# Performance work log

Measured on AMD Instinct MI355X. Metric: run time of the kernel, lower is better.

Reference implementation:

```python
import jax, jax.numpy as jnp
import numpy as np

N = 50000        # nodes
E = 800000       # edges (before self-loops)
IN = 128         # in_channels
HID = 256        # hidden_channels
HEADS = 8
C = HID // HEADS # per-head channels = 32
NC = 64          # num_classes
L = 3            # num_layers - 1 hidden GATConv layers


def setup_inputs() -> dict:
    key = jax.random.key(0)
    ks = jax.random.split(key, 12)
    x = jax.random.normal(ks[0], (N, IN), dtype=jnp.float32)
    edge_index = jax.random.randint(ks[1], (2, E), 0, N, dtype=jnp.int64)
    s = 0.05
    W0 = jax.random.normal(ks[2], (IN, HID), jnp.float32) * s
    b0 = jnp.zeros((HID,), jnp.float32)
    Wc = jax.random.normal(ks[3], (L, HID, HID), jnp.float32) * s
    a_src_c = jax.random.normal(ks[4], (L, HEADS, C), jnp.float32) * s
    a_dst_c = jax.random.normal(ks[5], (L, HEADS, C), jnp.float32) * s
    bc = jnp.zeros((L, HID), jnp.float32)
    Wl = jax.random.normal(ks[6], (HID, NC), jnp.float32) * s
    a_src_l = jax.random.normal(ks[7], (1, NC), jnp.float32) * s
    a_dst_l = jax.random.normal(ks[8], (1, NC), jnp.float32) * s
    bl = jnp.zeros((NC,), jnp.float32)
    return {"x": x, "edge_index": edge_index, "W0": W0, "b0": b0,
            "Wc": Wc, "a_src_c": a_src_c, "a_dst_c": a_dst_c, "bc": bc,
            "Wl": Wl, "a_src_l": a_src_l, "a_dst_l": a_dst_l, "bl": bl}


def gat_layer(h_in, W, a_s, a_d, b, src, dst, n, heads, c, concat):
    # PyG GATConv: h = x W -> [n, heads, c]
    h = (h_in @ W).reshape(n, heads, c)
    alpha_s = jnp.einsum('nhc,hc->nh', h, a_s)  # [n, heads]
    alpha_d = jnp.einsum('nhc,hc->nh', h, a_d)
    e = jax.nn.leaky_relu(alpha_s[src] + alpha_d[dst], 0.2)  # [E', heads]
    # scatter-softmax over incoming edges of each destination node
    m = jax.ops.segment_max(e, dst, num_segments=n)
    ex = jnp.exp(e - m[dst])
    den = jax.ops.segment_sum(ex, dst, num_segments=n)
    att = ex / (den[dst] + 1e-16)                            # [E', heads]
    out = jax.ops.segment_sum(h[src] * att[:, :, None], dst, num_segments=n)
    out = out.reshape(n, heads * c) if concat else out.mean(axis=1)
    return out + b


def reference(x, edge_index, W0, b0, Wc, a_src_c, a_dst_c, bc, Wl, a_src_l, a_dst_l, bl):
    n = x.shape[0]
    loops = jnp.arange(n, dtype=edge_index.dtype)
    src = jnp.concatenate([edge_index[0], loops])  # GATConv adds self-loops
    dst = jnp.concatenate([edge_index[1], loops])
    h = x @ W0 + b0                                 # node_embed
    xs = [h]
    for l in range(Wc.shape[0]):
        h = gat_layer(h, Wc[l], a_src_c[l], a_dst_c[l], bc[l], src, dst, n, HEADS, C, True)
        h = jax.nn.relu(h)                          # dropout p=0 (eval)
        xs.append(h)
    out = gat_layer(h, Wl, a_src_l, a_dst_l, bl, src, dst, n, 1, NC, False)
    xs.append(out)
    return jnp.concatenate(xs, axis=-1)             # JumpingKnowledge 'cat'
```

## Files before the change

kernel.cpp:

```cpp
#include <hip/hip_runtime.h>

typedef __attribute__((ext_vector_type(8))) short short8v;
typedef __attribute__((ext_vector_type(4))) float f32x4;

#define IN_CH 128
#define HID   256
#define HEADS 8
#define NCLS  64
#define LDO   1088
#define LDOU  2176

__device__ __forceinline__ unsigned short f2b(float f) {
    unsigned u = __float_as_uint(f);
    u += 0x7FFFu + ((u >> 16) & 1u);
    return (unsigned short)(u >> 16);
}
__device__ __forceinline__ float b2f(unsigned short s) {
    return __uint_as_float(((unsigned)s) << 16);
}

__global__ void detect64(const int* __restrict__ ei, int* __restrict__ flag, int E) {
    __shared__ int nz;
    if (threadIdx.x == 0) nz = 0;
    __syncthreads();
    int v = ei[2 * threadIdx.x + 1];
    if (v != 0) atomicAdd(&nz, 1);
    __syncthreads();
    if (threadIdx.x == 0) flag[0] = (nz == 0) ? 1 : 0;
}

__global__ void hist_k(const int* __restrict__ ei, const int* __restrict__ flag,
                       int* __restrict__ deg, int E) {
    int i = blockIdx.x * 256 + threadIdx.x;
    if (i >= E) return;
    int is64 = flag[0];
    int dst = is64 ? ei[2 * (E + i)] : ei[E + i];
    atomicAdd(&deg[dst], 1);
}

__global__ void scan_k(const int* __restrict__ deg, int* __restrict__ rowptr, int N) {
    __shared__ int sums[1024];
    int t = threadIdx.x;
    int chunk = (N + 1023) >> 10;
    int beg = t * chunk;
    int end = beg + chunk; if (end > N) end = N;
    if (beg > N) beg = N;
    int s = 0;
    for (int i = beg; i < end; ++i) s += deg[i];
    sums[t] = s;
    __syncthreads();
    for (int o = 1; o < 1024; o <<= 1) {
        int v = (t >= o) ? sums[t - o] : 0;
        __syncthreads();
        sums[t] += v;
        __syncthreads();
    }
    int run = (t == 0) ? 0 : sums[t - 1];
    for (int i = beg; i < end; ++i) { rowptr[i] = run; run += deg[i]; }
    if (t == 1023) rowptr[N] = sums[1023];
}

__global__ void fill_k(const int* __restrict__ ei, const int* __restrict__ flag,
                       const int* __restrict__ rowptr, int* __restrict__ cnt,
                       int* __restrict__ colb, int E) {
    int i = blockIdx.x * 256 + threadIdx.x;
    if (i >= E) return;
    int is64 = flag[0];
    int src, dst;
    if (is64) { src = ei[2 * i]; dst = ei[2 * (E + i)]; }
    else      { src = ei[i];     dst = ei[E + i]; }
    int pos = rowptr[dst] + atomicAdd(&cnt[dst], 1);
    colb[pos] = src;
}

__global__ void convtw(const float* __restrict__ W, unsigned short* __restrict__ WT,
                       int K, int N) {
    int i = blockIdx.x * 256 + threadIdx.x;
    if (i >= K * N) return;
    int k = i / N, n = i - k * N;
    WT[(size_t)n * K + k] = f2b(W[i]);
}

#define GBM 128
#define GBN 64
#define GBK 32
#define GLD 56

template<int OUTF32>
__global__ __launch_bounds__(256) void gemm_bf16(
    const float* __restrict__ A, int lda,
    const unsigned short* __restrict__ BT,
    int M, int N, int K,
    float* __restrict__ outF, const float* __restrict__ bias,
    unsigned short* __restrict__ outB, int ostride)
{
    __shared__ unsigned short Asm[GBM][GLD];
    __shared__ unsigned short Bsm[GBN][GLD];
    const int t = threadIdx.x;
    const int wid = t >> 6, lane = t & 63;
    const int m0 = blockIdx.x * GBM;
    const int n0 = blockIdx.y * GBN;
    const int wm = (wid >> 1) * 64;
    const int wn = (wid & 1) * 32;

    f32x4 acc[4][2];
#pragma unroll
    for (int i = 0; i < 4; ++i)
#pragma unroll
        for (int j = 0; j < 2; ++j) acc[i][j] = (f32x4)0.f;

    const int ar = t >> 3;
    const int ac = (t & 7) * 4;
    const int bc_ = t >> 2;
    const int bk = (t & 3) * 8;
    const int kk = (lane >> 4) * 8;
    const int rA = lane & 15;

    for (int k0 = 0; k0 < K; k0 += GBK) {
        __syncthreads();
#pragma unroll
        for (int p = 0; p < 4; ++p) {
            int row = ar + p * 32;
            int grow = m0 + row;
            float4 v = make_float4(0.f, 0.f, 0.f, 0.f);
            if (grow < M) v = *(const float4*)(A + (size_t)grow * lda + k0 + ac);
            ushort4 w4;
            w4.x = f2b(v.x); w4.y = f2b(v.y); w4.z = f2b(v.z); w4.w = f2b(v.w);
            *(ushort4*)&Asm[row][ac] = w4;
        }
        {
            int4 v = *(const int4*)(BT + (size_t)(n0 + bc_) * K + k0 + bk);
            *(int4*)&Bsm[bc_][bk] = v;
        }
        __syncthreads();
        short8v af[4], bfr[2];
#pragma unroll
        for (int i = 0; i < 4; ++i) af[i] = *(const short8v*)&Asm[wm + i * 16 + rA][kk];
#pragma unroll
        for (int j = 0; j < 2; ++j) bfr[j] = *(const short8v*)&Bsm[wn + j * 16 + rA][kk];
#pragma unroll
        for (int i = 0; i < 4; ++i)
#pragma unroll
            for (int j = 0; j < 2; ++j)
                acc[i][j] = __builtin_amdgcn_mfma_f32_16x16x32_bf16(af[i], bfr[j], acc[i][j], 0, 0, 0);
    }

    const int cr = (lane >> 4) * 4;
    const int cc = lane & 15;
#pragma unroll
    for (int i = 0; i < 4; ++i)
#pragma unroll
        for (int j = 0; j < 2; ++j)
#pragma unroll
            for (int r = 0; r < 4; ++r) {
                int row = m0 + wm + i * 16 + cr + r;
                int col = n0 + wn + j * 16 + cc;
                if (row < M) {
                    float v = acc[i][j][r];
                    if (OUTF32) outF[(size_t)row * LDO + col] = v + bias[col];
                    else        outB[(size_t)row * ostride + col] = f2b(v);
                }
            }
}

__global__ void alpha8(const unsigned short* __restrict__ tb, int tstride,
                       const float* __restrict__ as_, const float* __restrict__ ad_,
                       float* __restrict__ aS, float* __restrict__ aD, int n) {
    int wid = threadIdx.x >> 6, lane = threadIdx.x & 63;
    int node = blockIdx.x * 4 + wid;
    if (node >= n) return;
    int c = lane * 4;
    ushort4 hv = *(const ushort4*)(tb + (size_t)node * tstride + c);
    float4 av = *(const float4*)(as_ + c);
    float4 dv = *(const float4*)(ad_ + c);
    float h0 = b2f(hv.x), h1 = b2f(hv.y), h2 = b2f(hv.z), h3 = b2f(hv.w);
    float s = h0 * av.x + h1 * av.y + h2 * av.z + h3 * av.w;
    float d = h0 * dv.x + h1 * dv.y + h2 * dv.z + h3 * dv.w;
    s += __shfl_xor(s, 1); s += __shfl_xor(s, 2); s += __shfl_xor(s, 4);
    d += __shfl_xor(d, 1); d += __shfl_xor(d, 2); d += __shfl_xor(d, 4);
    if ((lane & 7) == 0) {
        aS[node * HEADS + (lane >> 3)] = s;
        aD[node * HEADS + (lane >> 3)] = d;
    }
}

__global__ void alpha1(const unsigned short* __restrict__ tb64, int tstride,
                       const float* __restrict__ as_, const float* __restrict__ ad_,
                       float* __restrict__ aS, float* __restrict__ aD, int n) {
    int wid = threadIdx.x >> 6, lane = threadIdx.x & 63;
    int node = blockIdx.x * 4 + wid;
    if (node >= n) return;
    float v = b2f(tb64[(size_t)node * tstride + lane]);
    float s = v * as_[lane], d = v * ad_[lane];
#pragma unroll
    for (int o = 1; o < 64; o <<= 1) { s += __shfl_xor(s, o); d += __shfl_xor(d, o); }
    if (lane == 0) { aS[node] = s; aD[node] = d; }
}

__global__ void agg8(const int* __restrict__ rowptr, const int* __restrict__ colb,
                     const float* __restrict__ aS, const float* __restrict__ aD,
                     const unsigned short* __restrict__ tb, int tstride,
                     const float* __restrict__ bias,
                     float* __restrict__ outp, int n, int dorelu) {
    int wid = threadIdx.x >> 6, lane = threadIdx.x & 63;
    int node = blockIdx.x * 4 + wid;
    if (node >= n) return;
    int c = lane * 4, head = lane >> 3;
    float aDv = aD[node * HEADS + head];
    float xs = aS[node * HEADS + head] + aDv;
    xs = xs > 0.f ? xs : 0.2f * xs;
    float wS = __expf(xs);
    float den = wS + 1e-16f;
    ushort4 hv0 = *(const ushort4*)(tb + (size_t)node * tstride + c);
    float a0 = wS * b2f(hv0.x), a1 = wS * b2f(hv0.y);
    float a2 = wS * b2f(hv0.z), a3 = wS * b2f(hv0.w);
    int s0 = rowptr[node], s1 = rowptr[node + 1];
    for (int e = s0; e < s1; ++e) {
        int src = colb[e];
        float xx = aS[src * HEADS + head] + aDv;
        xx = xx > 0.f ? xx : 0.2f * xx;
        float w = __expf(xx);
        den += w;
        ushort4 hv = *(const ushort4*)(tb + (size_t)src * tstride + c);
        a0 += w * b2f(hv.x); a1 += w * b2f(hv.y);
        a2 += w * b2f(hv.z); a3 += w * b2f(hv.w);
    }
    float inv = 1.f / den;
    float4 bv = *(const float4*)(bias + c);
    float o0 = a0 * inv + bv.x, o1 = a1 * inv + bv.y;
    float o2 = a2 * inv + bv.z, o3 = a3 * inv + bv.w;
    if (dorelu) {
        o0 = fmaxf(o0, 0.f); o1 = fmaxf(o1, 0.f);
        o2 = fmaxf(o2, 0.f); o3 = fmaxf(o3, 0.f);
    }
    *(float4*)(outp + (size_t)node * LDO + c) = make_float4(o0, o1, o2, o3);
}

__global__ void agg1(const int* __restrict__ rowptr, const int* __restrict__ colb,
                     const float* __restrict__ aS, const float* __restrict__ aD,
                     const unsigned short* __restrict__ tb64, int tstride,
                     const float* __restrict__ bl,
                     float* __restrict__ outp, int n) {
    int wid = threadIdx.x >> 6, lane = threadIdx.x & 63;
    int node = blockIdx.x * 4 + wid;
    if (node >= n) return;
    float aDv = aD[node];
    float xs = aS[node] + aDv;
    xs = xs > 0.f ? xs : 0.2f * xs;
    float wS = __expf(xs);
    float den = wS + 1e-16f;
    float acc = wS * b2f(tb64[(size_t)node * tstride + lane]);
    int s0 = rowptr[node], s1 = rowptr[node + 1];
    for (int e = s0; e < s1; ++e) {
        int src = colb[e];
        float xx = aS[src] + aDv;
        xx = xx > 0.f ? xx : 0.2f * xx;
        float w = __expf(xx);
        den += w;
        acc += w * b2f(tb64[(size_t)src * tstride + lane]);
    }
    outp[(size_t)node * LDO + 1024 + lane] = acc / den + bl[lane];
}

extern "C" void kernel_launch(void* const* d_in, const int* in_sizes, int n_in,
                              void* d_out, int out_size, void* d_ws, size_t ws_size,
                              hipStream_t stream) {
    const float* x   = (const float*)d_in[0];
    const int*   ei  = (const int*)d_in[1];
    const float* W0  = (const float*)d_in[2];
    const float* b0  = (const float*)d_in[3];
    const float* Wc  = (const float*)d_in[4];
    const float* asc = (const float*)d_in[5];
    const float* adc = (const float*)d_in[6];
    const float* bc  = (const float*)d_in[7];
    const float* Wl  = (const float*)d_in[8];
    const float* asl = (const float*)d_in[9];
    const float* adl = (const float*)d_in[10];
    const float* bl  = (const float*)d_in[11];
    float* out = (float*)d_out;
    unsigned short* outU = (unsigned short*)d_out;

    const int N = in_sizes[0] / IN_CH;
    const int E = in_sizes[1] / 2;

    unsigned short* t0 = outU + 896 * 2;
    unsigned short* t1 = outU + 768 * 2;
    unsigned short* t2 = outU;
    unsigned short* tF = outU + 128 * 2;

    char* ws = (char*)d_ws;
    size_t off = 0;
    auto take = [&](size_t bytes) -> void* {
        void* p = ws + off;
        off += (bytes + 255) & ~(size_t)255;
        return p;
    };
    unsigned short* WbT = (unsigned short*)take((size_t)245760 * 2);
    float* aS   = (float*)take((size_t)N * HEADS * 4);
    float* aD   = (float*)take((size_t)N * HEADS * 4);
    int* deg    = (int*)take((size_t)N * 4);
    int* cnt    = (int*)take((size_t)N * 4);
    int* rowptr = (int*)take((size_t)(N + 1) * 4);
    int* colb   = (int*)take((size_t)E * 4);
    int* flag   = (int*)take(256);

    unsigned short* W0T  = WbT;
    unsigned short* WcT0 = WbT + 32768;
    unsigned short* WlT  = WbT + 32768 + 3 * 65536;

    hipMemsetAsync(deg, 0, (size_t)N * 4, stream);
    hipMemsetAsync(cnt, 0, (size_t)N * 4, stream);

    detect64<<<1, 256, 0, stream>>>(ei, flag, E);
    convtw<<<(32768 + 255) / 256, 256, 0, stream>>>(W0, W0T, 128, 256);
    for (int l = 0; l < 3; ++l)
        convtw<<<(65536 + 255) / 256, 256, 0, stream>>>(Wc + l * 65536, WcT0 + l * 65536, 256, 256);
    convtw<<<(16384 + 255) / 256, 256, 0, stream>>>(Wl, WlT, 256, 64);

    hist_k<<<(E + 255) / 256, 256, 0, stream>>>(ei, flag, deg, E);
    scan_k<<<1, 1024, 0, stream>>>(deg, rowptr, N);
    fill_k<<<(E + 255) / 256, 256, 0, stream>>>(ei, flag, rowptr, cnt, colb, E);

    const int gmx = (N + GBM - 1) / GBM;
    const int nwb = (N + 3) / 4;

    gemm_bf16<1><<<dim3(gmx, 4), 256, 0, stream>>>(x, IN_CH, W0T, N, 256, 128, out, b0, nullptr, 0);

    unsigned short* tbs[3] = { t0, t1, t2 };
    for (int l = 0; l < 3; ++l) {
        gemm_bf16<0><<<dim3(gmx, 4), 256, 0, stream>>>(out + 256 * l, LDO, WcT0 + l * 65536,
                                                       N, 256, 256, nullptr, nullptr, tbs[l], LDOU);
        alpha8<<<nwb, 256, 0, stream>>>(tbs[l], LDOU, asc + l * 256, adc + l * 256, aS, aD, N);
        agg8<<<nwb, 256, 0, stream>>>(rowptr, colb, aS, aD, tbs[l], LDOU, bc + l * 256,
                                      out + 256 * (l + 1), N, 1);
    }

    gemm_bf16<0><<<dim3(gmx, 1), 256, 0, stream>>>(out + 768, LDO, WlT, N, 64, 256, nullptr, nullptr, tF, LDOU);
    alpha1<<<nwb, 256, 0, stream>>>(tF, LDOU, asl, adl, aS, aD, N);
    agg1<<<nwb, 256, 0, stream>>>(rowptr, colb, aS, aD, tF, LDOU, bl, out, N);

    gemm_bf16<1><<<dim3(gmx, 4), 256, 0, stream>>>(x, IN_CH, W0T, N, 256, 128, out, b0, nullptr, 0);
}
```

Before: 976.0 us.

## Feed GEMMs bf16 activations staged in output scratch and merge weight conversions

Layer outputs are now also written as bf16 copies into unused regions of the output buffer, and x is pre-converted to bf16, so the hidden-layer GEMMs read half-width bf16 A operands instead of converting fp32 in every tile. The GEMM K-tile is raised from 32 to 64. The five weight-transpose launches are merged into one kernel, and the aggregation loops get unroll hints. This cuts A-operand read traffic and launch count, but adds extra bf16 stores and relies on a careful aliasing plan for the scratch regions inside the output buffer.

Result: faster. 867.4 us (-11.1%).

```diff
diff --git a/kernel.cpp b/kernel.cpp
--- a/kernel.cpp
+++ b/kernel.cpp
@@ -73,24 +73,46 @@
     colb[pos] = src;
 }
 
-__global__ void convtw(const float* __restrict__ W, unsigned short* __restrict__ WT,
-                       int K, int N) {
+__global__ void convw_all(const float* __restrict__ W0, const float* __restrict__ Wc,
+                          const float* __restrict__ Wl,
+                          unsigned short* __restrict__ W0T, unsigned short* __restrict__ WcT,
+                          unsigned short* __restrict__ WlT) {
     int i = blockIdx.x * 256 + threadIdx.x;
-    if (i >= K * N) return;
-    int k = i / N, n = i - k * N;
-    WT[(size_t)n * K + k] = f2b(W[i]);
+    if (i < 32768) {
+        int k = i >> 8, n = i & 255;
+        W0T[n * 128 + k] = f2b(W0[i]);
+    } else if (i < 229376) {
+        int j = i - 32768;
+        int l = j >> 16, r = j & 65535;
+        int k = r >> 8, n = r & 255;
+        WcT[l * 65536 + n * 256 + k] = f2b(Wc[j]);
+    } else if (i < 245760) {
+        int j = i - 229376;
+        int k = j >> 6, n = j & 63;
+        WlT[n * 256 + k] = f2b(Wl[j]);
+    }
+}
+
+__global__ void convx(const float* __restrict__ x, unsigned short* __restrict__ xb, int n) {
+    int idx = blockIdx.x * 256 + threadIdx.x;
+    int node = idx >> 5, c = (idx & 31) * 4;
+    if (node >= n) return;
+    float4 v = *(const float4*)(x + (size_t)node * IN_CH + c);
+    ushort4 w;
+    w.x = f2b(v.x); w.y = f2b(v.y); w.z = f2b(v.z); w.w = f2b(v.w);
+    *(ushort4*)(xb + (size_t)node * LDOU + c) = w;
 }
 
 #define GBM 128
 #define GBN 64
-#define GBK 32
-#define GLD 56
-
-template<int OUTF32>
+#define GBK 64
+#define GLD 72
+
+template<int AF32, int MODE>
 __global__ __launch_bounds__(256) void gemm_bf16(
-    const float* __restrict__ A, int lda,
+    const void* __restrict__ Av, int lda,
     const unsigned short* __restrict__ BT,
-    int M, int N, int K,
+    int M, int K,
     float* __restrict__ outF, const float* __restrict__ bias,
     unsigned short* __restrict__ outB, int ostride)
 {
@@ -109,40 +131,57 @@
 #pragma unroll
         for (int j = 0; j < 2; ++j) acc[i][j] = (f32x4)0.f;
 
-    const int ar = t >> 3;
-    const int ac = (t & 7) * 4;
-    const int bc_ = t >> 2;
-    const int bk = (t & 3) * 8;
-    const int kk = (lane >> 4) * 8;
     const int rA = lane & 15;
+    const int kk8 = (lane >> 4) * 8;
 
     for (int k0 = 0; k0 < K; k0 += GBK) {
         __syncthreads();
-#pragma unroll
-        for (int p = 0; p < 4; ++p) {
-            int row = ar + p * 32;
-            int grow = m0 + row;
-            float4 v = make_float4(0.f, 0.f, 0.f, 0.f);
-            if (grow < M) v = *(const float4*)(A + (size_t)grow * lda + k0 + ac);
-            ushort4 w4;
-            w4.x = f2b(v.x); w4.y = f2b(v.y); w4.z = f2b(v.z); w4.w = f2b(v.w);
-            *(ushort4*)&Asm[row][ac] = w4;
+        if (AF32) {
+            const float* A = (const float*)Av;
+#pragma unroll
+            for (int p = 0; p < 8; ++p) {
+                int idx = p * 256 + t;
+                int row = idx >> 4, c4 = (idx & 15) * 4;
+                int grow = m0 + row;
+                float4 v = make_float4(0.f, 0.f, 0.f, 0.f);
+                if (grow < M) v = *(const float4*)(A + (size_t)grow * lda + k0 + c4);
+                ushort4 w;
+                w.x = f2b(v.x); w.y = f2b(v.y); w.z = f2b(v.z); w.w = f2b(v.w);
+                *(ushort4*)&Asm[row][c4] = w;
+            }
+        } else {
+            const unsigned short* A = (const unsigned short*)Av;
+#pragma unroll
+            for (int p = 0; p < 4; ++p) {
+                int idx = p * 256 + t;
+                int row = idx >> 3, ch = (idx & 7) * 8;
+                int grow = m0 + row;
+                int4 v = make_int4(0, 0, 0, 0);
+                if (grow < M) v = *(const int4*)(A + (size_t)grow * lda + k0 + ch);
+                *(int4*)&Asm[row][ch] = v;
+            }
         }
-        {
-            int4 v = *(const int4*)(BT + (size_t)(n0 + bc_) * K + k0 + bk);
-            *(int4*)&Bsm[bc_][bk] = v;
+#pragma unroll
+        for (int p = 0; p < 2; ++p) {
+            int idx = p * 256 + t;
+            int row = idx >> 3, ch = (idx & 7) * 8;
+            int4 v = *(const int4*)(BT + (size_t)(n0 + row) * K + k0 + ch);
+            *(int4*)&Bsm[row][ch] = v;
         }
         __syncthreads();
-        short8v af[4], bfr[2];
-#pragma unroll
-        for (int i = 0; i < 4; ++i) af[i] = *(const short8v*)&Asm[wm + i * 16 + rA][kk];
-#pragma unroll
-        for (int j = 0; j < 2; ++j) bfr[j] = *(const short8v*)&Bsm[wn + j * 16 + rA][kk];
-#pragma unroll
-        for (int i = 0; i < 4; ++i)
-#pragma unroll
-            for (int j = 0; j < 2; ++j)
-                acc[i][j] = __builtin_amdgcn_mfma_f32_16x16x32_bf16(af[i], bfr[j], acc[i][j], 0, 0, 0);
+#pragma unroll
+        for (int s = 0; s < 2; ++s) {
+            short8v af[4], bfv[2];
+#pragma unroll
+            for (int i = 0; i < 4; ++i) af[i] = *(const short8v*)&Asm[wm + i * 16 + rA][s * 32 + kk8];
+#pragma unroll
+            for (int j = 0; j < 2; ++j) bfv[j] = *(const short8v*)&Bsm[wn + j * 16 + rA][s * 32 + kk8];
+#pragma unroll
+            for (int i = 0; i < 4; ++i)
+#pragma unroll
+                for (int j = 0; j < 2; ++j)
+                    acc[i][j] = __builtin_amdgcn_mfma_f32_16x16x32_bf16(af[i], bfv[j], acc[i][j], 0, 0, 0);
+        }
     }
 
     const int cr = (lane >> 4) * 4;
@@ -155,10 +194,14 @@
             for (int r = 0; r < 4; ++r) {
                 int row = m0 + wm + i * 16 + cr + r;
                 int col = n0 + wn + j * 16 + cc;
-                if (row < M) {
-                    float v = acc[i][j][r];
-                    if (OUTF32) outF[(size_t)row * LDO + col] = v + bias[col];
-                    else        outB[(size_t)row * ostride + col] = f2b(v);
+                if (row >= M) continue;
+                float v = acc[i][j][r];
+                if (MODE == 0) {
+                    outB[(size_t)row * ostride + col] = f2b(v);
+                } else {
+                    v += bias[col];
+                    outF[(size_t)row * LDO + col] = v;
+                    if (MODE == 2) outB[(size_t)row * ostride + col] = f2b(v);
                 }
             }
 }
@@ -201,7 +244,8 @@
                      const float* __restrict__ aS, const float* __restrict__ aD,
                      const unsigned short* __restrict__ tb, int tstride,
                      const float* __restrict__ bias,
-                     float* __restrict__ outp, int n, int dorelu) {
+                     float* __restrict__ outp, unsigned short* __restrict__ outb,
+                     int n, int dorelu) {
     int wid = threadIdx.x >> 6, lane = threadIdx.x & 63;
     int node = blockIdx.x * 4 + wid;
     if (node >= n) return;
@@ -215,6 +259,7 @@
     float a0 = wS * b2f(hv0.x), a1 = wS * b2f(hv0.y);
     float a2 = wS * b2f(hv0.z), a3 = wS * b2f(hv0.w);
     int s0 = rowptr[node], s1 = rowptr[node + 1];
+#pragma unroll 2
     for (int e = s0; e < s1; ++e) {
         int src = colb[e];
         float xx = aS[src * HEADS + head] + aDv;
@@ -234,6 +279,9 @@
         o2 = fmaxf(o2, 0.f); o3 = fmaxf(o3, 0.f);
     }
     *(float4*)(outp + (size_t)node * LDO + c) = make_float4(o0, o1, o2, o3);
+    ushort4 ob;
+    ob.x = f2b(o0); ob.y = f2b(o1); ob.z = f2b(o2); ob.w = f2b(o3);
+    *(ushort4*)(outb + (size_t)node * LDOU + c) = ob;
 }
 
 __global__ void agg1(const int* __restrict__ rowptr, const int* __restrict__ colb,
@@ -251,6 +299,7 @@
     float den = wS + 1e-16f;
     float acc = wS * b2f(tb64[(size_t)node * tstride + lane]);
     int s0 = rowptr[node], s1 = rowptr[node + 1];
+#pragma unroll 2
     for (int e = s0; e < s1; ++e) {
         int src = colb[e];
         float xx = aS[src] + aDv;
@@ -283,11 +332,6 @@
     const int N = in_sizes[0] / IN_CH;
     const int E = in_sizes[1] / 2;
 
-    unsigned short* t0 = outU + 896 * 2;
-    unsigned short* t1 = outU + 768 * 2;
-    unsigned short* t2 = outU;
-    unsigned short* tF = outU + 128 * 2;
-
     char* ws = (char*)d_ws;
     size_t off = 0;
     auto take = [&](size_t bytes) -> void* {
@@ -304,18 +348,16 @@
     int* colb   = (int*)take((size_t)E * 4);
     int* flag   = (int*)take(256);
 
-    unsigned short* W0T  = WbT;
-    unsigned short* WcT0 = WbT + 32768;
-    unsigned short* WlT  = WbT + 32768 + 3 * 65536;
+    unsigned short* W0T = WbT;
+    unsigned short* WcT = WbT + 32768;
+    unsigned short* WlT = WbT + 32768 + 3 * 65536;
 
     hipMemsetAsync(deg, 0, (size_t)N * 4, stream);
     hipMemsetAsync(cnt, 0, (size_t)N * 4, stream);
 
     detect64<<<1, 256, 0, stream>>>(ei, flag, E);
-    convtw<<<(32768 + 255) / 256, 256, 0, stream>>>(W0, W0T, 128, 256);
-    for (int l = 0; l < 3; ++l)
-        convtw<<<(65536 + 255) / 256, 256, 0, stream>>>(Wc + l * 65536, WcT0 + l * 65536, 256, 256);
-    convtw<<<(16384 + 255) / 256, 256, 0, stream>>>(Wl, WlT, 256, 64);
+    convw_all<<<960, 256, 0, stream>>>(W0, Wc, Wl, W0T, WcT, WlT);
+    convx<<<(N * 32 + 255) / 256, 256, 0, stream>>>(x, outU + 512, N);
 
     hist_k<<<(E + 255) / 256, 256, 0, stream>>>(ei, flag, deg, E);
     scan_k<<<1, 1024, 0, stream>>>(deg, rowptr, N);
@@ -324,20 +366,25 @@
     const int gmx = (N + GBM - 1) / GBM;
     const int nwb = (N + 3) / 4;
 
-    gemm_bf16<1><<<dim3(gmx, 4), 256, 0, stream>>>(x, IN_CH, W0T, N, 256, 128, out, b0, nullptr, 0);
-
-    unsigned short* tbs[3] = { t0, t1, t2 };
+    gemm_bf16<0, 2><<<dim3(gmx, 4), 256, 0, stream>>>(outU + 512, LDOU, W0T, N, 128,
+                                                      out, b0, outU + 768, LDOU);
+
+    const unsigned short* Ab[3] = { outU + 768, outU + 1024, outU + 1792 };
+    unsigned short* tbs[3]      = { outU + 1792, outU + 1536, outU };
+    unsigned short* hb[3]       = { outU + 1024, outU + 1792, outU + 256 };
     for (int l = 0; l < 3; ++l) {
-        gemm_bf16<0><<<dim3(gmx, 4), 256, 0, stream>>>(out + 256 * l, LDO, WcT0 + l * 65536,
-                                                       N, 256, 256, nullptr, nullptr, tbs[l], LDOU);
+        gemm_bf16<0, 0><<<dim3(gmx, 4), 256, 0, stream>>>(Ab[l], LDOU, WcT + l * 65536, N, 256,
+                                                          nullptr, nullptr, tbs[l], LDOU);
         alpha8<<<nwb, 256, 0, stream>>>(tbs[l], LDOU, asc + l * 256, adc + l * 256, aS, aD, N);
         agg8<<<nwb, 256, 0, stream>>>(rowptr, colb, aS, aD, tbs[l], LDOU, bc + l * 256,
-                                      out + 256 * (l + 1), N, 1);
-    }
-
-    gemm_bf16<0><<<dim3(gmx, 1), 256, 0, stream>>>(out + 768, LDO, WlT, N, 64, 256, nullptr, nullptr, tF, LDOU);
-    alpha1<<<nwb, 256, 0, stream>>>(tF, LDOU, asl, adl, aS, aD, N);
-    agg1<<<nwb, 256, 0, stream>>>(rowptr, colb, aS, aD, tF, LDOU, bl, out, N);
-
-    gemm_bf16<1><<<dim3(gmx, 4), 256, 0, stream>>>(x, IN_CH, W0T, N, 256, 128, out, b0, nullptr, 0);
-}
+                                      out + 256 * (l + 1), hb[l], N, 1);
+    }
+
+    gemm_bf16<0, 0><<<dim3(gmx, 1), 256, 0, stream>>>(outU + 256, LDOU, WlT, N, 256,
+                                                      nullptr, nullptr, outU, LDOU);
+    alpha1<<<nwb, 256, 0, stream>>>(outU, LDOU, asl, adl, aS, aD, N);
+    agg1<<<nwb, 256, 0, stream>>>(rowptr, colb, aS, aD, outU, LDOU, bl, out, N);
+
+    gemm_bf16<1, 1><<<dim3(gmx, 4), 256, 0, stream>>>(x, IN_CH, W0T, N, 128,
+                                                      out, b0, nullptr, 0);
+}
```
